# Kernel tuning notes

Hardware: AMD Instinct MI355X
Metric: run time of the kernel (lower is better)

## Reference

```python
import jax, jax.numpy as jnp
import numpy as np

GROUPS = 32
HEADS = 4
EPS_GN = 1e-5
EPS_DEN = 1e-6


def group_norm(x, gamma, beta):
    b, c, h, w = x.shape
    xg = x.reshape(b, GROUPS, (c // GROUPS) * h * w)
    mu = xg.mean(axis=-1, keepdims=True)
    var = xg.var(axis=-1, keepdims=True)
    xn = ((xg - mu) * jax.lax.rsqrt(var + EPS_GN)).reshape(b, c, h, w)
    return xn * gamma[None, :, None, None] + beta[None, :, None, None]


def setup_inputs() -> dict:
    key = jax.random.key(0)
    ks = jax.random.split(key, 4)
    b, c, h, w = 16, 256, 64, 64
    x = jax.random.normal(ks[0], (b, c, h, w), dtype=jnp.float32)
    gamma = jnp.ones((c,), jnp.float32)
    beta = jnp.zeros((c,), jnp.float32)
    w_qkv = jax.random.normal(ks[1], (3 * c, c), jnp.float32) * (1.0 / np.sqrt(c))
    b_qkv = jnp.zeros((3 * c,), jnp.float32)
    w_out = jax.random.normal(ks[2], (c, c), jnp.float32) * (1.0 / np.sqrt(c))
    b_out = jnp.zeros((c,), jnp.float32)
    return {"x": x, "gamma": gamma, "beta": beta, "w_qkv": w_qkv,
            "b_qkv": b_qkv, "w_out": w_out, "b_out": b_out}


def reference(x, gamma, beta, w_qkv, b_qkv, w_out, b_out):
    b, c, h, w = x.shape
    d = c // HEADS
    n = h * w
    xn = group_norm(x, gamma, beta)
    # 1x1 conv == channel GEMM: [b,3c,h,w]
    qkv = jnp.einsum('bchw,oc->bohw', xn, w_qkv) + b_qkv[None, :, None, None]
    q, k, v = jnp.split(qkv, 3, axis=1)
    # b (heads d) h w -> b heads d n
    q = q.reshape(b, HEADS, d, n)
    k = k.reshape(b, HEADS, d, n)
    v = v.reshape(b, HEADS, d, n)
    q = jax.nn.elu(q) + 1.0
    k = jax.nn.elu(k) + 1.0
    k_sum = k.sum(axis=-1)                                 # [b,H,d]
    kv = jnp.einsum('bhdn,bhen->bhde', k, v)               # [b,H,d,d]
    out = jnp.einsum('bhde,bhdn->bhen', kv, q)             # [b,H,d,n]
    denom = jnp.einsum('bhdn,bhd->bhn', q, k_sum)          # [b,H,n]
    out = out / (denom[:, :, None, :] + EPS_DEN)
    out = out.reshape(b, c, h, w)
    out = jnp.einsum('bchw,oc->bohw', out, w_out) + b_out[None, :, None, None]
    return out + x
```

## Files before the change

### kernel.cpp

```cpp
#include <hip/hip_runtime.h>
#include <hip/hip_bf16.h>
#include <stdint.h>

#define BATCH 16
#define CH    256
#define NSP   4096
#define NH    4
#define HD    64

typedef __attribute__((ext_vector_type(8))) short bf16x8;
typedef __attribute__((ext_vector_type(4))) float f32x4;
typedef __attribute__((ext_vector_type(4))) unsigned int u32x4;

__device__ __forceinline__ short f2bf(float f) {
    __hip_bfloat16 h = __float2bfloat16(f);
    union { __hip_bfloat16 h; short s; } u; u.h = h;
    return u.s;
}
__device__ __forceinline__ float bf2f(short s) {
    union { float f; unsigned u; } v; v.u = ((unsigned)(unsigned short)s) << 16;
    return v.f;
}

__global__ __launch_bounds__(256) void k_pre(
        const float* __restrict__ x, const float* __restrict__ wq, const float* __restrict__ wo,
        float* __restrict__ mu, float* __restrict__ rstd,
        short* __restrict__ wq_bf, short* __restrict__ wo_bf) {
    int bg = blockIdx.x;
    if (bg < 512) {
        const float4* p = (const float4*)(x + (size_t)bg * 32768);
        float s = 0.f, sq = 0.f;
        for (int i = threadIdx.x; i < 8192; i += 256) {
            float4 v = p[i];
            s  += v.x + v.y + v.z + v.w;
            sq += v.x * v.x + v.y * v.y + v.z * v.z + v.w * v.w;
        }
        for (int off = 32; off; off >>= 1) { s += __shfl_down(s, off); sq += __shfl_down(sq, off); }
        __shared__ float ls[4], lq[4];
        int w = threadIdx.x >> 6;
        if ((threadIdx.x & 63) == 0) { ls[w] = s; lq[w] = sq; }
        __syncthreads();
        if (threadIdx.x == 0) {
            float S = ls[0] + ls[1] + ls[2] + ls[3];
            float Q = lq[0] + lq[1] + lq[2] + lq[3];
            float m = S / 32768.f;
            float var = Q / 32768.f - m * m;
            mu[bg] = m; rstd[bg] = rsqrtf(var + 1e-5f);
        }
    } else {
        int idx = ((bg - 512) * 256 + threadIdx.x) * 4;
        float4 v;
        short* dst;
        if (idx < 196608) { v = *(const float4*)(wq + idx); dst = wq_bf + idx; }
        else              { v = *(const float4*)(wo + (idx - 196608)); dst = wo_bf + (idx - 196608); }
        unsigned p0 = ((unsigned)(unsigned short)f2bf(v.x)) | (((unsigned)(unsigned short)f2bf(v.y)) << 16);
        unsigned p1 = ((unsigned)(unsigned short)f2bf(v.z)) | (((unsigned)(unsigned short)f2bf(v.w)) << 16);
        uint2 pk; pk.x = p0; pk.y = p1;
        *(uint2*)dst = pk;
    }
}

__global__ __launch_bounds__(256) void k_gnqkv(
        const float* __restrict__ x, const float* __restrict__ gamma, const float* __restrict__ beta,
        const float* __restrict__ mu, const float* __restrict__ rstd,
        const short* __restrict__ wq_bf, const float* __restrict__ b_qkv,
        short* __restrict__ q_t, short* __restrict__ kvp_bf, float* __restrict__ ksp) {
    int b = blockIdx.y, nt = blockIdx.x;
    int n0 = nt * 64;
    __shared__ short Blds[64 * 264];
    __shared__ union UR {
        struct { short kst[64 * 72]; short vst[64 * 72]; } s;
        short cst[64 * 136];
    } R;
    int t = threadIdx.x, lane = t & 63, wv = t >> 6, lr = lane & 15, quad = lane >> 4;

    {
        const float* xb = x + (size_t)b * CH * NSP;
        int m = t & 15, cq = t >> 4;
        for (int cb = 0; cb < 16; cb++) {
            int c = cb * 16 + cq;
            int g = c >> 3;
            float sc = rstd[b * 32 + g] * gamma[c];
            float sh = beta[c] - mu[b * 32 + g] * sc;
            float4 v = *(const float4*)(xb + (size_t)c * NSP + n0 + m * 4);
            float vv[4] = {v.x, v.y, v.z, v.w};
            #pragma unroll
            for (int j = 0; j < 4; j++) {
                int n = m * 4 + j;
                int cc = c ^ (((n >> 4) & 3) << 3);
                Blds[n * 264 + cc] = f2bf(vv[j] * sc + sh);
            }
        }
    }
    __syncthreads();

    for (int h = 0; h < 4; h++) {
        int base_row = (wv < 2 ? 256 : 512) + h * 64;
        int sub = (wv & 1) * 32;
        f32x4 acc[2][4] = {};
        for (int k0 = 0; k0 < 256; k0 += 32) {
            bf16x8 afr[2], bfr[4];
            #pragma unroll
            for (int mi = 0; mi < 2; mi++)
                afr[mi] = *(const bf16x8*)(wq_bf + (size_t)(base_row + sub + mi * 16 + lr) * 256 + k0 + quad * 8);
            #pragma unroll
            for (int ni = 0; ni < 4; ni++) {
                int rr = ni * 16 + lr;
                bfr[ni] = *(const bf16x8*)(Blds + rr * 264 + ((k0 + quad * 8) ^ (((rr >> 4) & 3) << 3)));
            }
            #pragma unroll
            for (int mi = 0; mi < 2; mi++)
                #pragma unroll
                for (int ni = 0; ni < 4; ni++)
                    acc[mi][ni] = __builtin_amdgcn_mfma_f32_16x16x32_bf16(afr[mi], bfr[ni], acc[mi][ni], 0, 0, 0);
        }
        __syncthreads();
        short* dst = (wv < 2) ? R.s.kst : R.s.vst;
        bool is_k = (wv < 2);
        #pragma unroll
        for (int mi = 0; mi < 2; mi++)
          #pragma unroll
          for (int ni = 0; ni < 4; ni++)
            #pragma unroll
            for (int r = 0; r < 4; r++) {
                int ol = sub + mi * 16 + quad * 4 + r;
                int nl = ni * 16 + lr;
                float v = acc[mi][ni][r] + b_qkv[base_row + ol];
                if (is_k) v = v > 0.f ? v + 1.f : __expf(v);
                dst[ol * 72 + nl] = f2bf(v);
            }
        __syncthreads();
        {
            int d = t >> 2, nq = (t & 3) * 16;
            float s = 0.f;
            #pragma unroll
            for (int j = 0; j < 16; j++) s += bf2f(R.s.kst[d * 72 + nq + j]);
            s += __shfl_down(s, 2);
            s += __shfl_down(s, 1);
            if ((t & 3) == 0) ksp[((size_t)(b * 4 + h) * 64 + nt) * 64 + d] = s;
        }
        f32x4 acc2[4] = {};
        #pragma unroll
        for (int kk = 0; kk < 64; kk += 32) {
            bf16x8 af = *(const bf16x8*)(R.s.vst + (wv * 16 + lr) * 72 + kk + quad * 8);
            bf16x8 bfk[4];
            #pragma unroll
            for (int ni = 0; ni < 4; ni++)
                bfk[ni] = *(const bf16x8*)(R.s.kst + (ni * 16 + lr) * 72 + kk + quad * 8);
            #pragma unroll
            for (int ni = 0; ni < 4; ni++)
                acc2[ni] = __builtin_amdgcn_mfma_f32_16x16x32_bf16(af, bfk[ni], acc2[ni], 0, 0, 0);
        }
        short* kvdst = kvp_bf + ((size_t)(b * 4 + h) * 64 + nt) * 4096;
        #pragma unroll
        for (int ni = 0; ni < 4; ni++)
            #pragma unroll
            for (int r = 0; r < 4; r++)
                kvdst[(wv * 16 + quad * 4 + r) * 64 + ni * 16 + lr] = f2bf(acc2[ni][r]);
    }

    for (int mtq = 0; mtq < 2; mtq++) {
        f32x4 acc[2][4] = {};
        int wm = wv * 32;
        for (int k0 = 0; k0 < 256; k0 += 32) {
            bf16x8 afr[2], bfr[4];
            #pragma unroll
            for (int mi = 0; mi < 2; mi++)
                afr[mi] = *(const bf16x8*)(wq_bf + (size_t)(mtq * 128 + wm + mi * 16 + lr) * 256 + k0 + quad * 8);
            #pragma unroll
            for (int ni = 0; ni < 4; ni++) {
                int rr = ni * 16 + lr;
                bfr[ni] = *(const bf16x8*)(Blds + rr * 264 + ((k0 + quad * 8) ^ (((rr >> 4) & 3) << 3)));
            }
            #pragma unroll
            for (int mi = 0; mi < 2; mi++)
                #pragma unroll
                for (int ni = 0; ni < 4; ni++)
                    acc[mi][ni] = __builtin_amdgcn_mfma_f32_16x16x32_bf16(afr[mi], bfr[ni], acc[mi][ni], 0, 0, 0);
        }
        __syncthreads();
        #pragma unroll
        for (int mi = 0; mi < 2; mi++)
          #pragma unroll
          for (int ni = 0; ni < 4; ni++)
            #pragma unroll
            for (int r = 0; r < 4; r++) {
                int ol = wm + mi * 16 + quad * 4 + r;
                int nl = ni * 16 + lr;
                float v = acc[mi][ni][r] + b_qkv[mtq * 128 + ol];
                v = v > 0.f ? v + 1.f : __expf(v);
                R.cst[nl * 136 + ol] = f2bf(v);
            }
        __syncthreads();
        #pragma unroll
        for (int i = 0; i < 4; i++) {
            int ch = t + i * 256;
            int row = ch >> 4, o8 = (ch & 15) * 8;
            int hh = mtq * 2 + (o8 >> 6), d0 = o8 & 63;
            *(u32x4*)(q_t + ((size_t)(b * 4 + hh) * NSP + n0 + row) * HD + d0) =
                *(const u32x4*)(R.cst + row * 136 + o8);
        }
    }
}

__global__ __launch_bounds__(256) void k_kv_reduce(
        const short* __restrict__ kvp_bf, const float* __restrict__ ksp,
        short* __restrict__ kvT_bf, float* __restrict__ ksum_g) {
    int p = blockIdx.x, bh = blockIdx.y;
    int t = threadIdx.x, lane = t & 63, grp = t >> 6;
    int chunk = p * 64 + lane;
    const short* base = kvp_bf + (size_t)bh * 64 * 4096 + chunk * 8;
    float s[8] = {};
    for (int ntc = grp * 16; ntc < grp * 16 + 16; ntc++) {
        bf16x8 v = *(const bf16x8*)(base + (size_t)ntc * 4096);
        #pragma unroll
        for (int j = 0; j < 8; j++) s[j] += bf2f(v[j]);
    }
    __shared__ float red[4][64][8];
    if (grp) {
        #pragma unroll
        for (int j = 0; j < 8; j++) red[grp][lane][j] = s[j];
    }
    __syncthreads();
    if (grp == 0) {
        bf16x8 rv;
        #pragma unroll
        for (int j = 0; j < 8; j++) {
            float v = s[j] + red[1][lane][j] + red[2][lane][j] + red[3][lane][j];
            rv[j] = f2bf(v);
        }
        *(bf16x8*)(kvT_bf + (size_t)bh * 4096 + chunk * 8) = rv;
    }
    if (p == 0) {
        const float* kb = ksp + (size_t)bh * 64 * 64 + lane;
        float ss = 0.f;
        for (int ntc = grp * 16; ntc < grp * 16 + 16; ntc++) ss += kb[(size_t)ntc * 64];
        __syncthreads();
        red[grp][lane][0] = ss;
        __syncthreads();
        if (grp == 0) ksum_g[bh * 64 + lane] = ss + red[1][lane][0] + red[2][lane][0] + red[3][lane][0];
    }
}

__global__ __launch_bounds__(256, 4) void k_attn_out(
        const short* __restrict__ q_t, const short* __restrict__ kvT_bf,
        const float* __restrict__ ksum_g, const short* __restrict__ wo_bf,
        const float* __restrict__ b_out, const float* __restrict__ x,
        float* __restrict__ out) {
    int b = blockIdx.y, nt = blockIdx.x;
    int n0 = nt * 64;
    __shared__ short ql[64 * 68];
    __shared__ short kvl[64 * 68];
    __shared__ short Bh[64 * 68];
    __shared__ float dnp[4][64];
    int t = threadIdx.x, lane = t & 63, wv = t >> 6, lr = lane & 15, quad = lane >> 4;

    f32x4 aco[4][4] = {};
    int r0 = wv * 64;

    #pragma unroll 1
    for (int h = 0; h < 4; h++) {
        int bh = b * 4 + h;
        #pragma unroll
        for (int i = 0; i < 2; i++) {
            int ch = t + i * 256;
            int row = ch >> 3, dc = (ch & 7) * 8;
            *(u32x4*)(ql + row * 68 + dc) =
                *(const u32x4*)(q_t + ((size_t)bh * NSP + n0 + row) * HD + dc);
            *(u32x4*)(kvl + row * 68 + dc) =
                *(const u32x4*)(kvT_bf + (size_t)bh * 4096 + row * 64 + dc);
        }
        __syncthreads();
        {
            int n = t & 63, q0 = wv * 16;
            const float* ks = ksum_g + bh * 64 + q0;
            float s = 0.f;
            #pragma unroll
            for (int j = 0; j < 16; j += 8) {
                bf16x8 qv = *(const bf16x8*)(ql + n * 68 + q0 + j);
                #pragma unroll
                for (int u = 0; u < 8; u++) s += bf2f(qv[u]) * ks[j + u];
            }
            dnp[wv][n] = s;
        }
        f32x4 acc2[4] = {};
        int nr = wv * 16;
        #pragma unroll
        for (int kk = 0; kk < 64; kk += 32) {
            bf16x8 af = *(const bf16x8*)(ql + (nr + lr) * 68 + kk + quad * 8);
            bf16x8 bfr[4];
            #pragma unroll
            for (int ni = 0; ni < 4; ni++)
                bfr[ni] = *(const bf16x8*)(kvl + (ni * 16 + lr) * 68 + kk + quad * 8);
            #pragma unroll
            for (int ni = 0; ni < 4; ni++)
                acc2[ni] = __builtin_amdgcn_mfma_f32_16x16x32_bf16(af, bfr[ni], acc2[ni], 0, 0, 0);
        }
        __syncthreads();
        float dn[4];
        #pragma unroll
        for (int r = 0; r < 4; r++) {
            int n = nr + quad * 4 + r;
            dn[r] = 1.f / (dnp[0][n] + dnp[1][n] + dnp[2][n] + dnp[3][n] + 1e-6f);
        }
        #pragma unroll
        for (int ni = 0; ni < 4; ni++)
            #pragma unroll
            for (int r = 0; r < 4; r++) {
                int n = nr + quad * 4 + r;
                Bh[n * 68 + ni * 16 + lr] = f2bf(acc2[ni][r] * dn[r]);
            }
        __syncthreads();
        #pragma unroll
        for (int kk = 0; kk < 2; kk++) {
            bf16x8 A[4];
            #pragma unroll
            for (int mi = 0; mi < 4; mi++)
                A[mi] = *(const bf16x8*)(wo_bf + (size_t)(r0 + mi * 16 + lr) * 256 + h * 64 + kk * 32 + quad * 8);
            bf16x8 bfr[4];
            #pragma unroll
            for (int nj = 0; nj < 4; nj++)
                bfr[nj] = *(const bf16x8*)(Bh + (nj * 16 + lr) * 68 + kk * 32 + quad * 8);
            #pragma unroll
            for (int mi = 0; mi < 4; mi++)
                #pragma unroll
                for (int nj = 0; nj < 4; nj++)
                    aco[mi][nj] = __builtin_amdgcn_mfma_f32_16x16x32_bf16(A[mi], bfr[nj], aco[mi][nj], 0, 0, 0);
        }
    }

    #pragma unroll
    for (int mi = 0; mi < 4; mi++)
      #pragma unroll
      for (int nj = 0; nj < 4; nj++)
        #pragma unroll
        for (int r = 0; r < 4; r++) {
            int o = r0 + mi * 16 + quad * 4 + r;
            int nl = nj * 16 + lr;
            size_t idx = ((size_t)b * CH + o) * NSP + n0 + nl;
            out[idx] = aco[mi][nj][r] + b_out[o] + x[idx];
        }
}

extern "C" void kernel_launch(void* const* d_in, const int* in_sizes, int n_in,
                              void* d_out, int out_size, void* d_ws, size_t ws_size,
                              hipStream_t stream) {
    const float* x     = (const float*)d_in[0];
    const float* gamma = (const float*)d_in[1];
    const float* beta  = (const float*)d_in[2];
    const float* w_qkv = (const float*)d_in[3];
    const float* b_qkv = (const float*)d_in[4];
    const float* w_out = (const float*)d_in[5];
    const float* b_out = (const float*)d_in[6];
    float* out = (float*)d_out;

    char* ws = (char*)d_ws;
    size_t off = 0;
    float* mu     = (float*)(ws + off); off += 2048;
    float* rstd   = (float*)(ws + off); off += 2048;
    short* wq_bf  = (short*)(ws + off); off += (size_t)768 * 256 * 2;
    short* wo_bf  = (short*)(ws + off); off += (size_t)256 * 256 * 2;
    short* q_t    = (short*)(ws + off); off += (size_t)BATCH * NSP * CH * 2;
    short* kvp_bf = (short*)(ws + off); off += (size_t)64 * 64 * 4096 * 2;
    float* ksp    = (float*)(ws + off); off += (size_t)64 * 64 * 64 * 4;
    short* kvT_bf = (short*)(ws + off); off += (size_t)64 * 4096 * 2;
    float* ksum_g = (float*)(ws + off); off += (size_t)64 * 64 * 4;

    if (ws_size < off) return;

    k_pre<<<768, 256, 0, stream>>>(x, w_qkv, w_out, mu, rstd, wq_bf, wo_bf);
    k_gnqkv<<<dim3(64, 16), 256, 0, stream>>>(x, gamma, beta, mu, rstd, wq_bf, b_qkv, q_t, kvp_bf, ksp);
    k_kv_reduce<<<dim3(8, 64), 256, 0, stream>>>(kvp_bf, ksp, kvT_bf, ksum_g);
    k_attn_out<<<dim3(64, 16), 256, 0, stream>>>(q_t, kvT_bf, ksum_g, wo_bf, b_out, x, out);
}
```

Baseline: 259.3 us.

## Materialize normalized bf16 activations in stats kernel and read them in QKV GEMM

The group-norm stats kernel now makes a second pass over each group, applies the per-channel scale and shift, and writes a bf16 copy of the normalized input to workspace. The QKV kernel then loads that half-width bf16 tensor instead of fp32 x, and no longer does per-element normalization. This trades an extra 32 MB write plus a re-read of x (likely still in cache) for halving the bytes read in the GEMM kernel. A fallback path is kept when the workspace is too small, and the output kernel's occupancy hint is lowered from 4 to 3 waves per SIMD.

```diff
diff --git a/kernel.cpp b/kernel.cpp
--- a/kernel.cpp
+++ b/kernel.cpp
@@ -22,10 +22,12 @@
     return v.f;
 }
 
+template<int XN>
 __global__ __launch_bounds__(256) void k_pre(
         const float* __restrict__ x, const float* __restrict__ wq, const float* __restrict__ wo,
+        const float* __restrict__ gamma, const float* __restrict__ beta,
         float* __restrict__ mu, float* __restrict__ rstd,
-        short* __restrict__ wq_bf, short* __restrict__ wo_bf) {
+        short* __restrict__ wq_bf, short* __restrict__ wo_bf, short* __restrict__ xn_bf) {
     int bg = blockIdx.x;
     if (bg < 512) {
         const float4* p = (const float4*)(x + (size_t)bg * 32768);
@@ -37,6 +39,7 @@
         }
         for (int off = 32; off; off >>= 1) { s += __shfl_down(s, off); sq += __shfl_down(sq, off); }
         __shared__ float ls[4], lq[4];
+        __shared__ float sc8[8], sh8[8];
         int w = threadIdx.x >> 6;
         if ((threadIdx.x & 63) == 0) { ls[w] = s; lq[w] = sq; }
         __syncthreads();
@@ -45,7 +48,31 @@
             float Q = lq[0] + lq[1] + lq[2] + lq[3];
             float m = S / 32768.f;
             float var = Q / 32768.f - m * m;
-            mu[bg] = m; rstd[bg] = rsqrtf(var + 1e-5f);
+            float r = rsqrtf(var + 1e-5f);
+            mu[bg] = m; rstd[bg] = r;
+            ls[0] = m; lq[0] = r;
+        }
+        if (XN) {
+            __syncthreads();
+            if (threadIdx.x < 8) {
+                int g = bg & 31, c = g * 8 + threadIdx.x;
+                float scv = lq[0] * gamma[c];
+                sc8[threadIdx.x] = scv;
+                sh8[threadIdx.x] = beta[c] - ls[0] * scv;
+            }
+            __syncthreads();
+            short* dst = xn_bf + (size_t)bg * 32768;
+            for (int i = threadIdx.x; i < 8192; i += 256) {
+                float4 v = p[i];
+                int cl = i >> 10;
+                float sc = sc8[cl], sh = sh8[cl];
+                unsigned p0 = ((unsigned)(unsigned short)f2bf(v.x * sc + sh)) |
+                              (((unsigned)(unsigned short)f2bf(v.y * sc + sh)) << 16);
+                unsigned p1 = ((unsigned)(unsigned short)f2bf(v.z * sc + sh)) |
+                              (((unsigned)(unsigned short)f2bf(v.w * sc + sh)) << 16);
+                uint2 pk; pk.x = p0; pk.y = p1;
+                *(uint2*)(dst + (size_t)i * 4) = pk;
+            }
         }
     } else {
         int idx = ((bg - 512) * 256 + threadIdx.x) * 4;
@@ -60,9 +87,11 @@
     }
 }
 
+template<int USE_XN>
 __global__ __launch_bounds__(256) void k_gnqkv(
         const float* __restrict__ x, const float* __restrict__ gamma, const float* __restrict__ beta,
         const float* __restrict__ mu, const float* __restrict__ rstd,
+        const short* __restrict__ xn_bf,
         const short* __restrict__ wq_bf, const float* __restrict__ b_qkv,
         short* __restrict__ q_t, short* __restrict__ kvp_bf, float* __restrict__ ksp) {
     int b = blockIdx.y, nt = blockIdx.x;
@@ -74,7 +103,24 @@
     } R;
     int t = threadIdx.x, lane = t & 63, wv = t >> 6, lr = lane & 15, quad = lane >> 4;
 
-    {
+    if (USE_XN) {
+        const short* xb = xn_bf + (size_t)b * CH * NSP + n0;
+        int m = t & 15, cq = t >> 4;
+        #pragma unroll 4
+        for (int cb = 0; cb < 16; cb++) {
+            int c = cb * 16 + cq;
+            uint2 v = *(const uint2*)(xb + (size_t)c * NSP + m * 4);
+            short sv[4];
+            sv[0] = (short)(v.x & 0xffffu); sv[1] = (short)(v.x >> 16);
+            sv[2] = (short)(v.y & 0xffffu); sv[3] = (short)(v.y >> 16);
+            #pragma unroll
+            for (int j = 0; j < 4; j++) {
+                int n = m * 4 + j;
+                int cc = c ^ (((n >> 4) & 3) << 3);
+                Blds[n * 264 + cc] = sv[j];
+            }
+        }
+    } else {
         const float* xb = x + (size_t)b * CH * NSP;
         int m = t & 15, cq = t >> 4;
         for (int cb = 0; cb < 16; cb++) {
@@ -242,7 +288,7 @@
     }
 }
 
-__global__ __launch_bounds__(256, 4) void k_attn_out(
+__global__ __launch_bounds__(256, 3) void k_attn_out(
         const short* __restrict__ q_t, const short* __restrict__ kvT_bf,
         const float* __restrict__ ksum_g, const short* __restrict__ wo_bf,
         const float* __restrict__ b_out, const float* __restrict__ x,
@@ -365,11 +411,19 @@
     float* ksp    = (float*)(ws + off); off += (size_t)64 * 64 * 64 * 4;
     short* kvT_bf = (short*)(ws + off); off += (size_t)64 * 4096 * 2;
     float* ksum_g = (float*)(ws + off); off += (size_t)64 * 64 * 4;
-
-    if (ws_size < off) return;
-
-    k_pre<<<768, 256, 0, stream>>>(x, w_qkv, w_out, mu, rstd, wq_bf, wo_bf);
-    k_gnqkv<<<dim3(64, 16), 256, 0, stream>>>(x, gamma, beta, mu, rstd, wq_bf, b_qkv, q_t, kvp_bf, ksp);
+    size_t off_base = off;
+    short* xn_bf  = (short*)(ws + off); off += (size_t)BATCH * CH * NSP * 2;
+
+    if (ws_size < off_base) return;
+    bool use_xn = (ws_size >= off);
+
+    if (use_xn) {
+        k_pre<1><<<768, 256, 0, stream>>>(x, w_qkv, w_out, gamma, beta, mu, rstd, wq_bf, wo_bf, xn_bf);
+        k_gnqkv<1><<<dim3(64, 16), 256, 0, stream>>>(x, gamma, beta, mu, rstd, xn_bf, wq_bf, b_qkv, q_t, kvp_bf, ksp);
+    } else {
+        k_pre<0><<<768, 256, 0, stream>>>(x, w_qkv, w_out, gamma, beta, mu, rstd, wq_bf, wo_bf, xn_bf);
+        k_gnqkv<0><<<dim3(64, 16), 256, 0, stream>>>(x, gamma, beta, mu, rstd, xn_bf, wq_bf, b_qkv, q_t, kvp_bf, ksp);
+    }
     k_kv_reduce<<<dim3(8, 64), 256, 0, stream>>>(kvp_bf, ksp, kvT_bf, ksum_g);
     k_attn_out<<<dim3(64, 16), 256, 0, stream>>>(q_t, kvT_bf, ksum_g, wo_bf, b_out, x, out);
 }
```

After: 268.9 us. 1.04x slower.

## Split group-norm transpose into separate kernel and read bf16 operand from global

Applied to the files above, without the earlier changes.

Adds a k_xnt kernel that normalizes x, converts it to bf16 and writes a transposed [n, c] copy to workspace. The QKV kernel then reads its B operand straight from global/L2 instead of staging it in a 33KB LDS tile, which frees LDS so more blocks can be resident. The cost is an extra launch and a 32MB bf16 write plus reread. The path is taken only when the workspace is large enough, with the old path kept as a fallback. k_attn_out's launch bounds also drop from 4 to 3 blocks per CU, giving it more registers per thread.

```diff
diff --git a/kernel.cpp b/kernel.cpp
--- a/kernel.cpp
+++ b/kernel.cpp
@@ -60,21 +60,59 @@
     }
 }
 
+__global__ __launch_bounds__(256) void k_xnt(
+        const float* __restrict__ x, const float* __restrict__ gamma, const float* __restrict__ beta,
+        const float* __restrict__ mu, const float* __restrict__ rstd,
+        short* __restrict__ xn_t) {
+    int b = blockIdx.y, nt = blockIdx.x, n0 = nt * 64;
+    __shared__ short T[64 * 264];
+    int t = threadIdx.x;
+    const float* xb = x + (size_t)b * CH * NSP;
+    int m = t & 15, cq = t >> 4;
+    #pragma unroll 4
+    for (int cb = 0; cb < 16; cb++) {
+        int c = cb * 16 + cq;
+        int g = c >> 3;
+        float sc = rstd[b * 32 + g] * gamma[c];
+        float sh = beta[c] - mu[b * 32 + g] * sc;
+        float4 v = *(const float4*)(xb + (size_t)c * NSP + n0 + m * 4);
+        float vv[4] = {v.x, v.y, v.z, v.w};
+        #pragma unroll
+        for (int j = 0; j < 4; j++) {
+            int n = m * 4 + j;
+            int cc = c ^ (((n >> 4) & 3) << 3);
+            T[n * 264 + cc] = f2bf(vv[j] * sc + sh);
+        }
+    }
+    __syncthreads();
+    short* dst = xn_t + ((size_t)b * NSP + n0) * CH;
+    #pragma unroll
+    for (int i = 0; i < 8; i++) {
+        int ch = t + i * 256;
+        int row = ch >> 5, dc = (ch & 31) * 8;
+        int sdc = dc ^ (((row >> 4) & 3) << 3);
+        *(u32x4*)(dst + row * CH + dc) = *(const u32x4*)(T + row * 264 + sdc);
+    }
+}
+
+template<int USE_XN>
 __global__ __launch_bounds__(256) void k_gnqkv(
         const float* __restrict__ x, const float* __restrict__ gamma, const float* __restrict__ beta,
         const float* __restrict__ mu, const float* __restrict__ rstd,
+        const short* __restrict__ xn_t,
         const short* __restrict__ wq_bf, const float* __restrict__ b_qkv,
         short* __restrict__ q_t, short* __restrict__ kvp_bf, float* __restrict__ ksp) {
     int b = blockIdx.y, nt = blockIdx.x;
     int n0 = nt * 64;
-    __shared__ short Blds[64 * 264];
+    __shared__ short Blds[USE_XN ? 1 : 64 * 264];
     __shared__ union UR {
         struct { short kst[64 * 72]; short vst[64 * 72]; } s;
         short cst[64 * 136];
     } R;
     int t = threadIdx.x, lane = t & 63, wv = t >> 6, lr = lane & 15, quad = lane >> 4;
-
-    {
+    const short* xrow = xn_t + ((size_t)b * NSP + n0) * CH;
+
+    if (!USE_XN) {
         const float* xb = x + (size_t)b * CH * NSP;
         int m = t & 15, cq = t >> 4;
         for (int cb = 0; cb < 16; cb++) {
@@ -91,8 +129,8 @@
                 Blds[n * 264 + cc] = f2bf(vv[j] * sc + sh);
             }
         }
-    }
-    __syncthreads();
+        __syncthreads();
+    }
 
     for (int h = 0; h < 4; h++) {
         int base_row = (wv < 2 ? 256 : 512) + h * 64;
@@ -106,7 +144,10 @@
             #pragma unroll
             for (int ni = 0; ni < 4; ni++) {
                 int rr = ni * 16 + lr;
-                bfr[ni] = *(const bf16x8*)(Blds + rr * 264 + ((k0 + quad * 8) ^ (((rr >> 4) & 3) << 3)));
+                if (USE_XN)
+                    bfr[ni] = *(const bf16x8*)(xrow + (size_t)rr * CH + k0 + quad * 8);
+                else
+                    bfr[ni] = *(const bf16x8*)(Blds + rr * 264 + ((k0 + quad * 8) ^ (((rr >> 4) & 3) << 3)));
             }
             #pragma unroll
             for (int mi = 0; mi < 2; mi++)
@@ -170,7 +211,10 @@
             #pragma unroll
             for (int ni = 0; ni < 4; ni++) {
                 int rr = ni * 16 + lr;
-                bfr[ni] = *(const bf16x8*)(Blds + rr * 264 + ((k0 + quad * 8) ^ (((rr >> 4) & 3) << 3)));
+                if (USE_XN)
+                    bfr[ni] = *(const bf16x8*)(xrow + (size_t)rr * CH + k0 + quad * 8);
+                else
+                    bfr[ni] = *(const bf16x8*)(Blds + rr * 264 + ((k0 + quad * 8) ^ (((rr >> 4) & 3) << 3)));
             }
             #pragma unroll
             for (int mi = 0; mi < 2; mi++)
@@ -242,7 +286,7 @@
     }
 }
 
-__global__ __launch_bounds__(256, 4) void k_attn_out(
+__global__ __launch_bounds__(256, 3) void k_attn_out(
         const short* __restrict__ q_t, const short* __restrict__ kvT_bf,
         const float* __restrict__ ksum_g, const short* __restrict__ wo_bf,
         const float* __restrict__ b_out, const float* __restrict__ x,
@@ -365,11 +409,19 @@
     float* ksp    = (float*)(ws + off); off += (size_t)64 * 64 * 64 * 4;
     short* kvT_bf = (short*)(ws + off); off += (size_t)64 * 4096 * 2;
     float* ksum_g = (float*)(ws + off); off += (size_t)64 * 64 * 4;
-
-    if (ws_size < off) return;
+    size_t off_base = off;
+    short* xn_t   = (short*)(ws + off); off += (size_t)BATCH * NSP * CH * 2;
+
+    if (ws_size < off_base) return;
+    bool use_xn = (ws_size >= off);
 
     k_pre<<<768, 256, 0, stream>>>(x, w_qkv, w_out, mu, rstd, wq_bf, wo_bf);
-    k_gnqkv<<<dim3(64, 16), 256, 0, stream>>>(x, gamma, beta, mu, rstd, wq_bf, b_qkv, q_t, kvp_bf, ksp);
+    if (use_xn) {
+        k_xnt<<<dim3(64, 16), 256, 0, stream>>>(x, gamma, beta, mu, rstd, xn_t);
+        k_gnqkv<1><<<dim3(64, 16), 256, 0, stream>>>(x, gamma, beta, mu, rstd, xn_t, wq_bf, b_qkv, q_t, kvp_bf, ksp);
+    } else {
+        k_gnqkv<0><<<dim3(64, 16), 256, 0, stream>>>(x, gamma, beta, mu, rstd, xn_t, wq_bf, b_qkv, q_t, kvp_bf, ksp);
+    }
     k_kv_reduce<<<dim3(8, 64), 256, 0, stream>>>(kvp_bf, ksp, kvT_bf, ksum_g);
     k_attn_out<<<dim3(64, 16), 256, 0, stream>>>(q_t, kvT_bf, ksum_g, wo_bf, b_out, x, out);
 }
```

Result: slower. 328.3 us (+26.6%).

## Enlarge per-wave GEMM tiles in QKV kernel and reuse input LDS for Q staging

Applied to the files above, without the earlier changes.

The QKV kernel now computes 64x64 tiles per wave (4x4 MFMA accumulators) instead of 32x64. The K/V part covers two heads per pass, with the waves taking turns writing their head's results to LDS. The Q GEMM is done in one pass over all 256 channels, and its output is staged into the now-free Blds buffer with packed 8-byte writes, replacing the separate union staging area. This cuts the number of passes over the B tile from LDS and the number of weight-fragment loads, at the cost of more accumulator registers and lower occupancy. The launch-bounds occupancy hint for the attention-output kernel is also lowered from 4 to 3.

```diff
diff --git a/kernel.cpp b/kernel.cpp
--- a/kernel.cpp
+++ b/kernel.cpp
@@ -16,6 +16,9 @@
     __hip_bfloat16 h = __float2bfloat16(f);
     union { __hip_bfloat16 h; short s; } u; u.h = h;
     return u.s;
+}
+__device__ __forceinline__ unsigned pack2bf(float a, float b) {
+    return ((unsigned)(unsigned short)f2bf(a)) | (((unsigned)(unsigned short)f2bf(b)) << 16);
 }
 __device__ __forceinline__ float bf2f(short s) {
     union { float f; unsigned u; } v; v.u = ((unsigned)(unsigned short)s) << 16;
@@ -53,9 +56,7 @@
         short* dst;
         if (idx < 196608) { v = *(const float4*)(wq + idx); dst = wq_bf + idx; }
         else              { v = *(const float4*)(wo + (idx - 196608)); dst = wo_bf + (idx - 196608); }
-        unsigned p0 = ((unsigned)(unsigned short)f2bf(v.x)) | (((unsigned)(unsigned short)f2bf(v.y)) << 16);
-        unsigned p1 = ((unsigned)(unsigned short)f2bf(v.z)) | (((unsigned)(unsigned short)f2bf(v.w)) << 16);
-        uint2 pk; pk.x = p0; pk.y = p1;
+        uint2 pk; pk.x = pack2bf(v.x, v.y); pk.y = pack2bf(v.z, v.w);
         *(uint2*)dst = pk;
     }
 }
@@ -68,10 +69,8 @@
     int b = blockIdx.y, nt = blockIdx.x;
     int n0 = nt * 64;
     __shared__ short Blds[64 * 264];
-    __shared__ union UR {
-        struct { short kst[64 * 72]; short vst[64 * 72]; } s;
-        short cst[64 * 136];
-    } R;
+    __shared__ short kst[64 * 72];
+    __shared__ short vst[64 * 72];
     int t = threadIdx.x, lane = t & 63, wv = t >> 6, lr = lane & 15, quad = lane >> 4;
 
     {
@@ -94,111 +93,122 @@
     }
     __syncthreads();
 
-    for (int h = 0; h < 4; h++) {
-        int base_row = (wv < 2 ? 256 : 512) + h * 64;
-        int sub = (wv & 1) * 32;
-        f32x4 acc[2][4] = {};
+    #pragma unroll 1
+    for (int p = 0; p < 2; p++) {
+        int grow = (wv < 2 ? 256 : 512) + (2 * p + (wv & 1)) * 64;
+        bool is_k = (wv < 2);
+        f32x4 acc[4][4] = {};
         for (int k0 = 0; k0 < 256; k0 += 32) {
-            bf16x8 afr[2], bfr[4];
-            #pragma unroll
-            for (int mi = 0; mi < 2; mi++)
-                afr[mi] = *(const bf16x8*)(wq_bf + (size_t)(base_row + sub + mi * 16 + lr) * 256 + k0 + quad * 8);
+            bf16x8 afr[4], bfr[4];
+            #pragma unroll
+            for (int mi = 0; mi < 4; mi++)
+                afr[mi] = *(const bf16x8*)(wq_bf + (size_t)(grow + mi * 16 + lr) * 256 + k0 + quad * 8);
             #pragma unroll
             for (int ni = 0; ni < 4; ni++) {
                 int rr = ni * 16 + lr;
                 bfr[ni] = *(const bf16x8*)(Blds + rr * 264 + ((k0 + quad * 8) ^ (((rr >> 4) & 3) << 3)));
             }
             #pragma unroll
-            for (int mi = 0; mi < 2; mi++)
+            for (int mi = 0; mi < 4; mi++)
                 #pragma unroll
                 for (int ni = 0; ni < 4; ni++)
                     acc[mi][ni] = __builtin_amdgcn_mfma_f32_16x16x32_bf16(afr[mi], bfr[ni], acc[mi][ni], 0, 0, 0);
         }
         __syncthreads();
-        short* dst = (wv < 2) ? R.s.kst : R.s.vst;
-        bool is_k = (wv < 2);
-        #pragma unroll
-        for (int mi = 0; mi < 2; mi++)
-          #pragma unroll
-          for (int ni = 0; ni < 4; ni++)
-            #pragma unroll
-            for (int r = 0; r < 4; r++) {
-                int ol = sub + mi * 16 + quad * 4 + r;
-                int nl = ni * 16 + lr;
-                float v = acc[mi][ni][r] + b_qkv[base_row + ol];
-                if (is_k) v = v > 0.f ? v + 1.f : __expf(v);
-                dst[ol * 72 + nl] = f2bf(v);
-            }
-        __syncthreads();
-        {
-            int d = t >> 2, nq = (t & 3) * 16;
-            float s = 0.f;
-            #pragma unroll
-            for (int j = 0; j < 16; j++) s += bf2f(R.s.kst[d * 72 + nq + j]);
-            s += __shfl_down(s, 2);
-            s += __shfl_down(s, 1);
-            if ((t & 3) == 0) ksp[((size_t)(b * 4 + h) * 64 + nt) * 64 + d] = s;
-        }
-        f32x4 acc2[4] = {};
-        #pragma unroll
-        for (int kk = 0; kk < 64; kk += 32) {
-            bf16x8 af = *(const bf16x8*)(R.s.vst + (wv * 16 + lr) * 72 + kk + quad * 8);
-            bf16x8 bfk[4];
+        #pragma unroll 1
+        for (int hh = 0; hh < 2; hh++) {
+            int hp = 2 * p + hh;
+            if ((wv & 1) == hh) {
+                short* dst = is_k ? kst : vst;
+                #pragma unroll
+                for (int mi = 0; mi < 4; mi++)
+                  #pragma unroll
+                  for (int ni = 0; ni < 4; ni++)
+                    #pragma unroll
+                    for (int r = 0; r < 4; r++) {
+                        int ol = mi * 16 + quad * 4 + r;
+                        int nl = ni * 16 + lr;
+                        float v = acc[mi][ni][r] + b_qkv[grow + ol];
+                        if (is_k) v = v > 0.f ? v + 1.f : __expf(v);
+                        dst[ol * 72 + nl] = f2bf(v);
+                    }
+            }
+            __syncthreads();
+            {
+                int d = t >> 2, nq = (t & 3) * 16;
+                float s = 0.f;
+                #pragma unroll
+                for (int j = 0; j < 16; j++) s += bf2f(kst[d * 72 + nq + j]);
+                s += __shfl_down(s, 2);
+                s += __shfl_down(s, 1);
+                if ((t & 3) == 0) ksp[((size_t)(b * 4 + hp) * 64 + nt) * 64 + d] = s;
+            }
+            f32x4 acc2[4] = {};
+            #pragma unroll
+            for (int kk = 0; kk < 64; kk += 32) {
+                bf16x8 af = *(const bf16x8*)(vst + (wv * 16 + lr) * 72 + kk + quad * 8);
+                bf16x8 bfk[4];
+                #pragma unroll
+                for (int ni = 0; ni < 4; ni++)
+                    bfk[ni] = *(const bf16x8*)(kst + (ni * 16 + lr) * 72 + kk + quad * 8);
+                #pragma unroll
+                for (int ni = 0; ni < 4; ni++)
+                    acc2[ni] = __builtin_amdgcn_mfma_f32_16x16x32_bf16(af, bfk[ni], acc2[ni], 0, 0, 0);
+            }
+            short* kvdst = kvp_bf + ((size_t)(b * 4 + hp) * 64 + nt) * 4096;
             #pragma unroll
             for (int ni = 0; ni < 4; ni++)
-                bfk[ni] = *(const bf16x8*)(R.s.kst + (ni * 16 + lr) * 72 + kk + quad * 8);
-            #pragma unroll
-            for (int ni = 0; ni < 4; ni++)
-                acc2[ni] = __builtin_amdgcn_mfma_f32_16x16x32_bf16(af, bfk[ni], acc2[ni], 0, 0, 0);
-        }
-        short* kvdst = kvp_bf + ((size_t)(b * 4 + h) * 64 + nt) * 4096;
-        #pragma unroll
-        for (int ni = 0; ni < 4; ni++)
-            #pragma unroll
-            for (int r = 0; r < 4; r++)
-                kvdst[(wv * 16 + quad * 4 + r) * 64 + ni * 16 + lr] = f2bf(acc2[ni][r]);
-    }
-
-    for (int mtq = 0; mtq < 2; mtq++) {
-        f32x4 acc[2][4] = {};
-        int wm = wv * 32;
+                #pragma unroll
+                for (int r = 0; r < 4; r++)
+                    kvdst[(wv * 16 + quad * 4 + r) * 64 + ni * 16 + lr] = f2bf(acc2[ni][r]);
+            if (!(p == 1 && hh == 1)) __syncthreads();
+        }
+    }
+
+    {
+        int r0q = wv * 64;
+        f32x4 acc[4][4] = {};
         for (int k0 = 0; k0 < 256; k0 += 32) {
-            bf16x8 afr[2], bfr[4];
-            #pragma unroll
-            for (int mi = 0; mi < 2; mi++)
-                afr[mi] = *(const bf16x8*)(wq_bf + (size_t)(mtq * 128 + wm + mi * 16 + lr) * 256 + k0 + quad * 8);
+            bf16x8 afr[4], bfr[4];
+            #pragma unroll
+            for (int mi = 0; mi < 4; mi++)
+                afr[mi] = *(const bf16x8*)(wq_bf + (size_t)(r0q + mi * 16 + lr) * 256 + k0 + quad * 8);
             #pragma unroll
             for (int ni = 0; ni < 4; ni++) {
                 int rr = ni * 16 + lr;
                 bfr[ni] = *(const bf16x8*)(Blds + rr * 264 + ((k0 + quad * 8) ^ (((rr >> 4) & 3) << 3)));
             }
             #pragma unroll
-            for (int mi = 0; mi < 2; mi++)
+            for (int mi = 0; mi < 4; mi++)
                 #pragma unroll
                 for (int ni = 0; ni < 4; ni++)
                     acc[mi][ni] = __builtin_amdgcn_mfma_f32_16x16x32_bf16(afr[mi], bfr[ni], acc[mi][ni], 0, 0, 0);
         }
         __syncthreads();
         #pragma unroll
-        for (int mi = 0; mi < 2; mi++)
+        for (int mi = 0; mi < 4; mi++)
           #pragma unroll
-          for (int ni = 0; ni < 4; ni++)
-            #pragma unroll
-            for (int r = 0; r < 4; r++) {
-                int ol = wm + mi * 16 + quad * 4 + r;
+          for (int ni = 0; ni < 4; ni++) {
+                int ol0 = r0q + mi * 16 + quad * 4;
                 int nl = ni * 16 + lr;
-                float v = acc[mi][ni][r] + b_qkv[mtq * 128 + ol];
-                v = v > 0.f ? v + 1.f : __expf(v);
-                R.cst[nl * 136 + ol] = f2bf(v);
-            }
-        __syncthreads();
-        #pragma unroll
-        for (int i = 0; i < 4; i++) {
+                float v[4];
+                #pragma unroll
+                for (int r = 0; r < 4; r++) {
+                    float u = acc[mi][ni][r] + b_qkv[ol0 + r];
+                    v[r] = u > 0.f ? u + 1.f : __expf(u);
+                }
+                uint2 pk; pk.x = pack2bf(v[0], v[1]); pk.y = pack2bf(v[2], v[3]);
+                *(uint2*)(Blds + nl * 264 + ol0) = pk;
+          }
+        __syncthreads();
+        #pragma unroll
+        for (int i = 0; i < 8; i++) {
             int ch = t + i * 256;
-            int row = ch >> 4, o8 = (ch & 15) * 8;
-            int hh = mtq * 2 + (o8 >> 6), d0 = o8 & 63;
+            int row = ch >> 5;
+            int o8 = (ch & 31) * 8;
+            int hh = o8 >> 6, d0 = o8 & 63;
             *(u32x4*)(q_t + ((size_t)(b * 4 + hh) * NSP + n0 + row) * HD + d0) =
-                *(const u32x4*)(R.cst + row * 136 + o8);
+                *(const u32x4*)(Blds + row * 264 + o8);
         }
     }
 }
@@ -242,7 +252,7 @@
     }
 }
 
-__global__ __launch_bounds__(256, 4) void k_attn_out(
+__global__ __launch_bounds__(256, 3) void k_attn_out(
         const short* __restrict__ q_t, const short* __restrict__ kvT_bf,
         const float* __restrict__ ksum_g, const short* __restrict__ wo_bf,
         const float* __restrict__ b_out, const float* __restrict__ x,
```

Result: slower. 277.0 us (+6.8%).
